# Performance work log

Measured on AMD Instinct MI355X. Metric: run time of the kernel, lower is better.

The kernel has to match this reference:

```python
import jax, jax.numpy as jnp
import numpy as np

FINE_VOCAB = 1_000_000
COARSE_VOCAB = 10_000
D = 128          # embedding_dim
H = 32           # gate hidden width
B, L = 2048, 200 # batch, history length


def setup_inputs() -> dict:
    key = jax.random.key(0)
    ks = jax.random.split(key, 8)
    fine_ids = jax.random.randint(ks[0], (B, L), 0, FINE_VOCAB, dtype=jnp.int64)
    coarse_ids = jax.random.randint(ks[1], (B, L), 0, COARSE_VOCAB, dtype=jnp.int64)
    # embedding tables (xavier-ish scale); padding row 0 zeroed (padding_idx=0)
    fine_W = (jax.random.normal(ks[2], (FINE_VOCAB + 1, D), jnp.float32) * 0.02).at[0].set(0.0)
    coarse_W = (jax.random.normal(ks[3], (COARSE_VOCAB + 1, D), jnp.float32) * 0.02).at[0].set(0.0)
    # freq table initialized to ones, padding row zeroed
    freq_W = jnp.ones((FINE_VOCAB + 1, 1), jnp.float32).at[0].set(0.0)
    # gate MLP: Linear(2D+1 -> 32), ReLU, Linear(32 -> 1), Sigmoid
    W1 = jax.random.normal(ks[4], (2 * D + 1, H), jnp.float32) * (1.0 / np.sqrt(2 * D + 1))
    b1 = jnp.zeros((H,), jnp.float32)
    W2 = jax.random.normal(ks[5], (H, 1), jnp.float32) * (1.0 / np.sqrt(H))
    b2 = jnp.zeros((1,), jnp.float32)
    return {"fine_ids": fine_ids, "coarse_ids": coarse_ids, "fine_W": fine_W,
            "coarse_W": coarse_W, "freq_W": freq_W, "W1": W1, "b1": b1,
            "W2": W2, "b2": b2}


def reference(fine_ids, coarse_ids, fine_W, coarse_W, freq_W, W1, b1, W2, b2):
    fine_emb = fine_W[fine_ids]          # [B, L, D]
    coarse_emb = coarse_W[coarse_ids]    # [B, L, D]
    freq_weight = jax.nn.sigmoid(freq_W[fine_ids])  # [B, L, 1]
    combined = jnp.concatenate([fine_emb, coarse_emb, freq_weight], axis=-1)  # [B, L, 2D+1]
    h = jax.nn.relu(combined @ W1 + b1)                 # [B, L, H]
    gate = jax.nn.sigmoid(h @ W2 + b2)                  # [B, L, 1]
    adjusted_gate = gate * freq_weight                  # [B, L, 1]
    fused = adjusted_gate * fine_emb + (1.0 - adjusted_gate) * coarse_emb
    return fused, adjusted_gate
```

## Files before the change

kernel.cpp:

```cpp
#include <hip/hip_runtime.h>
#include <math.h>


#define DD 128
#define HH 32

typedef float  f32x4  __attribute__((ext_vector_type(4)));
typedef short  bf16x8 __attribute__((ext_vector_type(8)));

__device__ __forceinline__ float sigmoid_f(float x) {
    return 1.0f / (1.0f + expf(-x));
}

__device__ __forceinline__ unsigned short bf16_rne(float x) {
    union { float f; unsigned u; } c; c.f = x;
    unsigned u = c.u + 0x7fffu + ((c.u >> 16) & 1u);
    return (unsigned short)(u >> 16);
}

__global__ __launch_bounds__(256) void coarse_mlp_kernel(
    const float* __restrict__ coarse_W,
    const float* __restrict__ W1,
    const float* __restrict__ b1,
    float* __restrict__ hc,
    int nCoarse)
{
    const int t = blockIdx.x * 256 + threadIdx.x;
    if (t >= nCoarse * HH) return;
    const int r = t >> 5;
    const int j = t & 31;
    const float* __restrict__ row = coarse_W + (size_t)r * DD;
    const float* __restrict__ w   = W1 + DD * HH + j;
    float acc = b1[j];
    #pragma unroll 8
    for (int i = 0; i < DD; ++i)
        acc = fmaf(row[i], w[i * HH], acc);
    hc[t] = acc;
}

__global__ __launch_bounds__(256, 3) void fused_kernel(
    const int*   __restrict__ fine_ids,
    const int*   __restrict__ coarse_ids,
    const float* __restrict__ fine_W,
    const float* __restrict__ coarse_W,
    const float* __restrict__ freq_W,
    const float* __restrict__ W1,
    const float* __restrict__ W2,
    const float* __restrict__ b2,
    const float* __restrict__ hc,
    float* __restrict__ out_fused,
    float* __restrict__ out_gate)
{
    __shared__ __align__(16) unsigned int sX[8192];
    __shared__ float s_adj[256];
    __shared__ float s_fw[256];
    __shared__ int   s_if[256];
    __shared__ int   s_ic[256];

    const int tid  = threadIdx.x;
    const int lane = tid & 63;
    const int wave = tid >> 6;
    const int P0   = (int)blockIdx.x * 256;

    const int jlo = lane & 15;
    const int kg  = lane >> 4;

    {
        const int p = P0 + tid;
        const int idf = fine_ids[p];
        const int idc = coarse_ids[p];
        const float fr = freq_W[idf];
        s_if[tid] = idf;
        s_ic[tid] = idc;
        s_fw[tid] = sigmoid_f(fr);
    }

    bf16x8 bfr[2][4];
    #pragma unroll
    for (int n = 0; n < 2; ++n)
        #pragma unroll
        for (int ks = 0; ks < 4; ++ks)
            #pragma unroll
            for (int i = 0; i < 8; ++i) {
                const int k = ks * 32 + kg * 8 + i;
                bfr[n][ks][i] = (short)bf16_rne(W1[k * HH + jlo + 16 * n]);
            }

    const float w256_0 = W1[2 * DD * HH + jlo];
    const float w256_1 = W1[2 * DD * HH + jlo + 16];
    const float W2_0   = W2[jlo];
    const float W2_1   = W2[jlo + 16];
    const float b2v    = b2[0];

    __syncthreads();

    #pragma unroll 1
    for (int h = 0; h < 2; ++h) {
        const int hbase = h * 128;

        #pragma unroll 4
        for (int it = 0; it < 32; ++it) {
            const int rr  = wave * 32 + it;
            const int idf = s_if[hbase + rr];
            const float2 v = *(const float2*)(fine_W + (size_t)idf * DD + 2 * lane);
            const unsigned pk = (unsigned)bf16_rne(v.x)
                              | ((unsigned)bf16_rne(v.y) << 16);
            *(unsigned*)((char*)sX + rr * 256 + ((4 * lane) ^ ((rr & 7) << 4))) = pk;
        }
        __syncthreads();

        #pragma unroll 1
        for (int mt2 = 0; mt2 < 2; ++mt2) {
            const int mt    = wave * 2 + mt2;
            const int rbase = mt * 16;
            f32x4 acc0 = {0.f, 0.f, 0.f, 0.f};
            f32x4 acc1 = {0.f, 0.f, 0.f, 0.f};
            const int rr = rbase + jlo;
            #pragma unroll
            for (int ks = 0; ks < 4; ++ks) {
                const bf16x8 a = *(const bf16x8*)((const char*)sX
                    + rr * 256 + ((kg * 16 + ks * 64) ^ ((rr & 7) << 4)));
                acc0 = __builtin_amdgcn_mfma_f32_16x16x32_bf16(a, bfr[0][ks], acc0, 0, 0, 0);
                acc1 = __builtin_amdgcn_mfma_f32_16x16x32_bf16(a, bfr[1][ks], acc1, 0, 0, 0);
            }
            #pragma unroll
            for (int r = 0; r < 4; ++r) {
                const int posl = hbase + rbase + kg * 4 + r;
                const int idc  = s_ic[posl];
                const float fw = s_fw[posl];
                const float* __restrict__ hcrow = hc + idc * HH;
                const float v0 = acc0[r] + hcrow[jlo]      + w256_0 * fw;
                const float v1 = acc1[r] + hcrow[jlo + 16] + w256_1 * fw;
                float tr = fmaxf(v0, 0.f) * W2_0 + fmaxf(v1, 0.f) * W2_1;
                tr += __shfl_xor(tr, 1);
                tr += __shfl_xor(tr, 2);
                tr += __shfl_xor(tr, 4);
                tr += __shfl_xor(tr, 8);
                const float adj = sigmoid_f(tr + b2v) * fw;
                if (jlo == r) s_adj[posl] = adj;
            }
        }
        __syncthreads();
    }

    __builtin_nontemporal_store(s_adj[tid], out_gate + P0 + tid);

    const int half = lane >> 5;
    const int d0   = (lane & 31) * 4;
    const int waveBase = wave * 64;
    #pragma unroll 1
    for (int q = 0; q < 64; q += 2) {
        const int slot = waveBase + q + half;
        const float a  = s_adj[slot];
        const int   jf = s_if[slot] * DD;
        const int   jc = s_ic[slot] * DD;
        const float4 f = *(const float4*)(fine_W   + (size_t)jf + d0);
        const float4 c = *(const float4*)(coarse_W + (size_t)jc + d0);
        f32x4 o;
        o.x = fmaf(a, f.x - c.x, c.x);
        o.y = fmaf(a, f.y - c.y, c.y);
        o.z = fmaf(a, f.z - c.z, c.z);
        o.w = fmaf(a, f.w - c.w, c.w);
        f32x4* dst = (f32x4*)(out_fused + (size_t)(P0 + slot) * DD + d0);
        __builtin_nontemporal_store(o, dst);
    }
}

extern "C" void kernel_launch(void* const* d_in, const int* in_sizes, int n_in,
                              void* d_out, int out_size, void* d_ws, size_t ws_size,
                              hipStream_t stream) {
    const int*   fine_ids   = (const int*)  d_in[0];
    const int*   coarse_ids = (const int*)  d_in[1];
    const float* fine_W     = (const float*)d_in[2];
    const float* coarse_W   = (const float*)d_in[3];
    const float* freq_W     = (const float*)d_in[4];
    const float* W1         = (const float*)d_in[5];
    const float* b1         = (const float*)d_in[6];
    const float* W2         = (const float*)d_in[7];
    const float* b2         = (const float*)d_in[8];

    const int n       = in_sizes[0];
    const int nCoarse = in_sizes[3] / DD;

    float* out_fused = (float*)d_out;
    float* out_gate  = (float*)d_out + (size_t)n * DD;
    float* hc        = (float*)d_ws;

    coarse_mlp_kernel<<<dim3((nCoarse * HH + 255) / 256), dim3(256), 0, stream>>>(
        coarse_W, W1, b1, hc, nCoarse);

    fused_kernel<<<dim3(n / 256), dim3(256), 0, stream>>>(
        fine_ids, coarse_ids, fine_W, coarse_W, freq_W,
        W1, W2, b2, hc, out_fused, out_gate);
}
```

Before: 141.4 us.

## Double-buffer fine-embedding gather into LDS with register prefetch across chunks

The gate-MLP phase now runs over four 64-row chunks instead of two 128-row halves. The next chunk's fine-embedding rows are gathered into registers while the current chunk's MFMA and epilogue run, then written into a second LDS buffer. This is meant to hide the random-gather latency behind compute. Launch bounds also ask for 4 blocks per CU, which combined with the 16 float2 prefetch registers may force spills or limit occupancy.

```diff
diff --git a/kernel.cpp b/kernel.cpp
--- a/kernel.cpp
+++ b/kernel.cpp
@@ -38,7 +38,7 @@
     hc[t] = acc;
 }
 
-__global__ __launch_bounds__(256, 3) void fused_kernel(
+__global__ __launch_bounds__(256, 4) void fused_kernel(
     const int*   __restrict__ fine_ids,
     const int*   __restrict__ coarse_ids,
     const float* __restrict__ fine_W,
@@ -51,7 +51,7 @@
     float* __restrict__ out_fused,
     float* __restrict__ out_gate)
 {
-    __shared__ __align__(16) unsigned int sX[8192];
+    __shared__ __align__(16) unsigned int sX[2][4096];
     __shared__ float s_adj[256];
     __shared__ float s_fw[256];
     __shared__ int   s_if[256];
@@ -69,10 +69,9 @@
         const int p = P0 + tid;
         const int idf = fine_ids[p];
         const int idc = coarse_ids[p];
-        const float fr = freq_W[idf];
         s_if[tid] = idf;
         s_ic[tid] = idc;
-        s_fw[tid] = sigmoid_f(fr);
+        s_fw[tid] = sigmoid_f(freq_W[idf]);
     }
 
     bf16x8 bfr[2][4];
@@ -94,50 +93,69 @@
 
     __syncthreads();
 
+    float2 rv[16];
+    #pragma unroll
+    for (int it = 0; it < 16; ++it) {
+        const int rr  = wave * 16 + it;
+        const int idf = s_if[rr];
+        rv[it] = *(const float2*)(fine_W + (size_t)idf * DD + 2 * lane);
+    }
+    #pragma unroll
+    for (int it = 0; it < 16; ++it) {
+        const int rr = wave * 16 + it;
+        const unsigned pk = (unsigned)bf16_rne(rv[it].x)
+                          | ((unsigned)bf16_rne(rv[it].y) << 16);
+        *(unsigned*)((char*)&sX[0][0] + rr * 256 + ((4 * lane) ^ ((rr & 7) << 4))) = pk;
+    }
+    __syncthreads();
+
     #pragma unroll 1
-    for (int h = 0; h < 2; ++h) {
-        const int hbase = h * 128;
-
-        #pragma unroll 4
-        for (int it = 0; it < 32; ++it) {
-            const int rr  = wave * 32 + it;
-            const int idf = s_if[hbase + rr];
-            const float2 v = *(const float2*)(fine_W + (size_t)idf * DD + 2 * lane);
-            const unsigned pk = (unsigned)bf16_rne(v.x)
-                              | ((unsigned)bf16_rne(v.y) << 16);
-            *(unsigned*)((char*)sX + rr * 256 + ((4 * lane) ^ ((rr & 7) << 4))) = pk;
-        }
-        __syncthreads();
-
-        #pragma unroll 1
-        for (int mt2 = 0; mt2 < 2; ++mt2) {
-            const int mt    = wave * 2 + mt2;
-            const int rbase = mt * 16;
-            f32x4 acc0 = {0.f, 0.f, 0.f, 0.f};
-            f32x4 acc1 = {0.f, 0.f, 0.f, 0.f};
-            const int rr = rbase + jlo;
+    for (int c = 0; c < 4; ++c) {
+        if (c < 3) {
             #pragma unroll
-            for (int ks = 0; ks < 4; ++ks) {
-                const bf16x8 a = *(const bf16x8*)((const char*)sX
-                    + rr * 256 + ((kg * 16 + ks * 64) ^ ((rr & 7) << 4)));
-                acc0 = __builtin_amdgcn_mfma_f32_16x16x32_bf16(a, bfr[0][ks], acc0, 0, 0, 0);
-                acc1 = __builtin_amdgcn_mfma_f32_16x16x32_bf16(a, bfr[1][ks], acc1, 0, 0, 0);
+            for (int it = 0; it < 16; ++it) {
+                const int rr  = wave * 16 + it;
+                const int idf = s_if[(c + 1) * 64 + rr];
+                rv[it] = *(const float2*)(fine_W + (size_t)idf * DD + 2 * lane);
             }
+        }
+
+        const char* bufc = (const char*)&sX[c & 1][0];
+        f32x4 acc0 = {0.f, 0.f, 0.f, 0.f};
+        f32x4 acc1 = {0.f, 0.f, 0.f, 0.f};
+        const int rr = wave * 16 + jlo;
+        #pragma unroll
+        for (int ks = 0; ks < 4; ++ks) {
+            const bf16x8 a = *(const bf16x8*)(bufc
+                + rr * 256 + ((kg * 16 + ks * 64) ^ ((rr & 7) << 4)));
+            acc0 = __builtin_amdgcn_mfma_f32_16x16x32_bf16(a, bfr[0][ks], acc0, 0, 0, 0);
+            acc1 = __builtin_amdgcn_mfma_f32_16x16x32_bf16(a, bfr[1][ks], acc1, 0, 0, 0);
+        }
+        #pragma unroll
+        for (int r = 0; r < 4; ++r) {
+            const int posl = c * 64 + wave * 16 + kg * 4 + r;
+            const int idc  = s_ic[posl];
+            const float fw = s_fw[posl];
+            const float* __restrict__ hcrow = hc + idc * HH;
+            const float v0 = acc0[r] + hcrow[jlo]      + w256_0 * fw;
+            const float v1 = acc1[r] + hcrow[jlo + 16] + w256_1 * fw;
+            float tr = fmaxf(v0, 0.f) * W2_0 + fmaxf(v1, 0.f) * W2_1;
+            tr += __shfl_xor(tr, 1);
+            tr += __shfl_xor(tr, 2);
+            tr += __shfl_xor(tr, 4);
+            tr += __shfl_xor(tr, 8);
+            const float adj = sigmoid_f(tr + b2v) * fw;
+            if (jlo == r) s_adj[posl] = adj;
+        }
+
+        if (c < 3) {
+            char* dst = (char*)&sX[(c + 1) & 1][0];
             #pragma unroll
-            for (int r = 0; r < 4; ++r) {
-                const int posl = hbase + rbase + kg * 4 + r;
-                const int idc  = s_ic[posl];
-                const float fw = s_fw[posl];
-                const float* __restrict__ hcrow = hc + idc * HH;
-                const float v0 = acc0[r] + hcrow[jlo]      + w256_0 * fw;
-                const float v1 = acc1[r] + hcrow[jlo + 16] + w256_1 * fw;
-                float tr = fmaxf(v0, 0.f) * W2_0 + fmaxf(v1, 0.f) * W2_1;
-                tr += __shfl_xor(tr, 1);
-                tr += __shfl_xor(tr, 2);
-                tr += __shfl_xor(tr, 4);
-                tr += __shfl_xor(tr, 8);
-                const float adj = sigmoid_f(tr + b2v) * fw;
-                if (jlo == r) s_adj[posl] = adj;
+            for (int it = 0; it < 16; ++it) {
+                const int rr = wave * 16 + it;
+                const unsigned pk = (unsigned)bf16_rne(rv[it].x)
+                                  | ((unsigned)bf16_rne(rv[it].y) << 16);
+                *(unsigned*)(dst + rr * 256 + ((4 * lane) ^ ((rr & 7) << 4))) = pk;
             }
         }
         __syncthreads();
```

Result: no change. 140.2 us (-0.9%).

## Keep gathered fine rows in registers and run per-wave pipelines without block syncs

Applied to the files above, without the earlier changes.

The kernel now has each wave gather its own 16 fine-embedding rows into registers at a time. It converts them to bf16 in a per-wave LDS tile, runs the gate MFMA and writes the gate output. It then reuses the register copy of each fine row for the fused blend, instead of gathering fine_W a second time in a separate epilogue. This removes the block-wide __syncthreads and the s_adj staging, and shrinks LDS per block, so occupancy is raised to 4 blocks. The cost is more register pressure from holding 16 float2 rows, and output stores narrowing from float4 to float2 per lane.

```diff
diff --git a/kernel.cpp b/kernel.cpp
--- a/kernel.cpp
+++ b/kernel.cpp
@@ -5,6 +5,7 @@
 #define DD 128
 #define HH 32
 
+typedef float  f32x2  __attribute__((ext_vector_type(2)));
 typedef float  f32x4  __attribute__((ext_vector_type(4)));
 typedef short  bf16x8 __attribute__((ext_vector_type(8)));
 
@@ -38,7 +39,7 @@
     hc[t] = acc;
 }
 
-__global__ __launch_bounds__(256, 3) void fused_kernel(
+__global__ __launch_bounds__(256, 4) void fused_kernel(
     const int*   __restrict__ fine_ids,
     const int*   __restrict__ coarse_ids,
     const float* __restrict__ fine_W,
@@ -51,8 +52,7 @@
     float* __restrict__ out_fused,
     float* __restrict__ out_gate)
 {
-    __shared__ __align__(16) unsigned int sX[8192];
-    __shared__ float s_adj[256];
+    __shared__ __align__(16) unsigned int sX[4][1024];
     __shared__ float s_fw[256];
     __shared__ int   s_if[256];
     __shared__ int   s_ic[256];
@@ -68,11 +68,9 @@
     {
         const int p = P0 + tid;
         const int idf = fine_ids[p];
-        const int idc = coarse_ids[p];
-        const float fr = freq_W[idf];
         s_if[tid] = idf;
-        s_ic[tid] = idc;
-        s_fw[tid] = sigmoid_f(fr);
+        s_ic[tid] = coarse_ids[p];
+        s_fw[tid] = sigmoid_f(freq_W[idf]);
     }
 
     bf16x8 bfr[2][4];
@@ -92,77 +90,67 @@
     const float W2_1   = W2[jlo + 16];
     const float b2v    = b2[0];
 
-    __syncthreads();
+    char* const swave = (char*)&sX[wave][0];
+    const int wbase = wave * 64;
 
     #pragma unroll 1
-    for (int h = 0; h < 2; ++h) {
-        const int hbase = h * 128;
+    for (int it = 0; it < 4; ++it) {
+        const int base = wbase + it * 16;
 
-        #pragma unroll 4
-        for (int it = 0; it < 32; ++it) {
-            const int rr  = wave * 32 + it;
-            const int idf = s_if[hbase + rr];
-            const float2 v = *(const float2*)(fine_W + (size_t)idf * DD + 2 * lane);
-            const unsigned pk = (unsigned)bf16_rne(v.x)
-                              | ((unsigned)bf16_rne(v.y) << 16);
-            *(unsigned*)((char*)sX + rr * 256 + ((4 * lane) ^ ((rr & 7) << 4))) = pk;
+        float2 rv[16];
+        #pragma unroll
+        for (int i = 0; i < 16; ++i) {
+            const int idf = s_if[base + i];
+            rv[i] = *(const float2*)(fine_W + (size_t)idf * DD + 2 * lane);
         }
-        __syncthreads();
 
-        #pragma unroll 1
-        for (int mt2 = 0; mt2 < 2; ++mt2) {
-            const int mt    = wave * 2 + mt2;
-            const int rbase = mt * 16;
-            f32x4 acc0 = {0.f, 0.f, 0.f, 0.f};
-            f32x4 acc1 = {0.f, 0.f, 0.f, 0.f};
-            const int rr = rbase + jlo;
-            #pragma unroll
-            for (int ks = 0; ks < 4; ++ks) {
-                const bf16x8 a = *(const bf16x8*)((const char*)sX
-                    + rr * 256 + ((kg * 16 + ks * 64) ^ ((rr & 7) << 4)));
-                acc0 = __builtin_amdgcn_mfma_f32_16x16x32_bf16(a, bfr[0][ks], acc0, 0, 0, 0);
-                acc1 = __builtin_amdgcn_mfma_f32_16x16x32_bf16(a, bfr[1][ks], acc1, 0, 0, 0);
-            }
-            #pragma unroll
-            for (int r = 0; r < 4; ++r) {
-                const int posl = hbase + rbase + kg * 4 + r;
-                const int idc  = s_ic[posl];
-                const float fw = s_fw[posl];
-                const float* __restrict__ hcrow = hc + idc * HH;
-                const float v0 = acc0[r] + hcrow[jlo]      + w256_0 * fw;
-                const float v1 = acc1[r] + hcrow[jlo + 16] + w256_1 * fw;
-                float tr = fmaxf(v0, 0.f) * W2_0 + fmaxf(v1, 0.f) * W2_1;
-                tr += __shfl_xor(tr, 1);
-                tr += __shfl_xor(tr, 2);
-                tr += __shfl_xor(tr, 4);
-                tr += __shfl_xor(tr, 8);
-                const float adj = sigmoid_f(tr + b2v) * fw;
-                if (jlo == r) s_adj[posl] = adj;
-            }
+        #pragma unroll
+        for (int i = 0; i < 16; ++i) {
+            const unsigned pk = (unsigned)bf16_rne(rv[i].x)
+                              | ((unsigned)bf16_rne(rv[i].y) << 16);
+            *(unsigned*)(swave + i * 256 + ((4 * lane) ^ ((i & 7) << 4))) = pk;
         }
-        __syncthreads();
-    }
 
-    __builtin_nontemporal_store(s_adj[tid], out_gate + P0 + tid);
+        f32x4 acc0 = {0.f, 0.f, 0.f, 0.f};
+        f32x4 acc1 = {0.f, 0.f, 0.f, 0.f};
+        #pragma unroll
+        for (int ks = 0; ks < 4; ++ks) {
+            const bf16x8 a = *(const bf16x8*)(swave
+                + jlo * 256 + ((kg * 16 + ks * 64) ^ ((jlo & 7) << 4)));
+            acc0 = __builtin_amdgcn_mfma_f32_16x16x32_bf16(a, bfr[0][ks], acc0, 0, 0, 0);
+            acc1 = __builtin_amdgcn_mfma_f32_16x16x32_bf16(a, bfr[1][ks], acc1, 0, 0, 0);
+        }
 
-    const int half = lane >> 5;
-    const int d0   = (lane & 31) * 4;
-    const int waveBase = wave * 64;
-    #pragma unroll 1
-    for (int q = 0; q < 64; q += 2) {
-        const int slot = waveBase + q + half;
-        const float a  = s_adj[slot];
-        const int   jf = s_if[slot] * DD;
-        const int   jc = s_ic[slot] * DD;
-        const float4 f = *(const float4*)(fine_W   + (size_t)jf + d0);
-        const float4 c = *(const float4*)(coarse_W + (size_t)jc + d0);
-        f32x4 o;
-        o.x = fmaf(a, f.x - c.x, c.x);
-        o.y = fmaf(a, f.y - c.y, c.y);
-        o.z = fmaf(a, f.z - c.z, c.z);
-        o.w = fmaf(a, f.w - c.w, c.w);
-        f32x4* dst = (f32x4*)(out_fused + (size_t)(P0 + slot) * DD + d0);
-        __builtin_nontemporal_store(o, dst);
+        float adjv[4];
+        #pragma unroll
+        for (int r = 0; r < 4; ++r) {
+            const int posl = base + kg * 4 + r;
+            const int idc  = s_ic[posl];
+            const float fw = s_fw[posl];
+            const float* __restrict__ hcrow = hc + idc * HH;
+            const float v0 = acc0[r] + hcrow[jlo]      + w256_0 * fw;
+            const float v1 = acc1[r] + hcrow[jlo + 16] + w256_1 * fw;
+            float tr = fmaxf(v0, 0.f) * W2_0 + fmaxf(v1, 0.f) * W2_1;
+            tr += __shfl_xor(tr, 1);
+            tr += __shfl_xor(tr, 2);
+            tr += __shfl_xor(tr, 4);
+            tr += __shfl_xor(tr, 8);
+            adjv[r] = sigmoid_f(tr + b2v) * fw;
+            if (jlo == r)
+                __builtin_nontemporal_store(adjv[r], out_gate + P0 + posl);
+        }
+
+        #pragma unroll
+        for (int i = 0; i < 16; ++i) {
+            const float a = __shfl(adjv[i & 3], ((i >> 2) << 4) + (i & 3));
+            const int idc = s_ic[base + i];
+            const float2 c2 = *(const float2*)(coarse_W + (size_t)idc * DD + 2 * lane);
+            f32x2 o;
+            o.x = fmaf(a, rv[i].x - c2.x, c2.x);
+            o.y = fmaf(a, rv[i].y - c2.y, c2.y);
+            f32x2* dst = (f32x2*)(out_fused + (size_t)(P0 + base + i) * DD + 2 * lane);
+            __builtin_nontemporal_store(o, dst);
+        }
     }
 }
 
```

After: 118.2 us (median of 2 runs). -16.4%, faster.
